# Performance work log

Hardware: AMD Instinct MI355X
Metric: run time of the kernel (lower is better)

Reference implementation:

```python
import jax, jax.numpy as jnp
import numpy as np

D_MODEL = 1024
N_HEADS = 16
HEAD_DIM = D_MODEL // N_HEADS
B, T = 2, 2048


def setup_inputs() -> dict:
    key = jax.random.key(0)
    ks = jax.random.split(key, 6)
    x = jax.random.normal(ks[0], (B, T, D_MODEL), dtype=jnp.float32)
    tgt_key_padding_mask = jnp.zeros((B, T), dtype=bool)
    scale = 0.02
    Wq = jax.random.normal(ks[1], (D_MODEL, D_MODEL), dtype=jnp.float32) * scale
    Wk = jax.random.normal(ks[2], (D_MODEL, D_MODEL), dtype=jnp.float32) * scale
    Wv = jax.random.normal(ks[3], (D_MODEL, D_MODEL), dtype=jnp.float32) * scale
    Wo = jax.random.normal(ks[4], (D_MODEL, D_MODEL), dtype=jnp.float32) * scale
    return {"x": x, "tgt_key_padding_mask": tgt_key_padding_mask,
            "Wq": Wq, "Wk": Wk, "Wv": Wv, "Wo": Wo}


def reference(x, tgt_key_padding_mask, Wq, Wk, Wv, Wo):
    # Eval-mode (dropout disabled) masked causal MHA, faithful to torch module.
    b, t, c = x.shape
    h, d = N_HEADS, HEAD_DIM
    # nn.Linear(bias=False): y = x @ W.T
    Q = (x @ Wq.T).reshape(b, t, h, d).transpose(0, 2, 1, 3)  # [B,H,T,d]
    K = (x @ Wk.T).reshape(b, t, h, d).transpose(0, 2, 1, 3)
    V = (x @ Wv.T).reshape(b, t, h, d).transpose(0, 2, 1, 3)
    scores = jnp.einsum('bhqd,bhkd->bhqk', Q, K) / jnp.sqrt(jnp.float32(d))
    # causal mask: True above the diagonal -> -inf
    cmask = jnp.triu(jnp.ones((t, t), dtype=bool), k=1)  # [T,T]
    neg_inf = jnp.float32(-jnp.inf)
    scores = jnp.where(cmask[None, None, :, :], neg_inf, scores)
    # key padding mask: [B,T] True=PAD, broadcast over query dim
    pmask = tgt_key_padding_mask[:, None, None, :]  # [B,1,1,T]
    scores = jnp.where(pmask, neg_inf, scores)
    attn = jax.nn.softmax(scores, axis=-1)
    out = jnp.einsum('bhqk,bhkd->bhqd', attn, V)  # [B,H,T,d]
    out = out.transpose(0, 2, 1, 3).reshape(b, t, c)
    out = out @ Wo.T
    return out
```

## Files before the change

### kernel.cpp

```cpp
#include <hip/hip_runtime.h>
#include <hip/hip_bf16.h>
#include <stdint.h>

#define D_MODEL 1024
#define NHEADS  16
#define HDIM    64
#define BB      2
#define TT      2048
#define MROWS   (BB*TT)
#define GK      1024

typedef __bf16 bf16_8 __attribute__((ext_vector_type(8)));
typedef __bf16 bf16_4 __attribute__((ext_vector_type(4)));
typedef float  f32x4  __attribute__((ext_vector_type(4)));
typedef unsigned short u16;

__device__ __forceinline__ u16 f2bf(float f) {
    union { float f; uint32_t u; } c; c.f = f;
    uint32_t u = c.u;
    uint32_t r = (u + 0x7FFFu + ((u >> 16) & 1u)) >> 16;
    return (u16)r;
}
__device__ __forceinline__ uint32_t pk2bf(float a, float b) {
    return (uint32_t)f2bf(a) | ((uint32_t)f2bf(b) << 16);
}

__device__ __forceinline__ void gload16(const void* g, void* l) {
    __builtin_amdgcn_global_load_lds(
        (const __attribute__((address_space(1))) unsigned int*)g,
        (__attribute__((address_space(3))) unsigned int*)l,
        16, 0, 0);
}

__global__ __launch_bounds__(256) void cvtk(
    const float* __restrict__ x,  const float* __restrict__ wq,
    const float* __restrict__ wk, const float* __restrict__ wv,
    const float* __restrict__ wo, const unsigned char* __restrict__ mk,
    u16* __restrict__ xb,  u16* __restrict__ wqb, u16* __restrict__ wkb,
    u16* __restrict__ wvb, u16* __restrict__ wob, uint32_t* __restrict__ pmb)
{
    int z = blockIdx.y;
    if (z == 5) {
        int gi = blockIdx.x*256 + threadIdx.x;
        if (gi < BB*TT/32) {
            uint32_t wv = 0;
            #pragma unroll
            for (int j = 0; j < 32; ++j)
                wv |= (mk[gi*32 + j] ? 1u : 0u) << j;
            pmb[gi] = wv;
        }
        return;
    }
    const float* in; u16* out; int n4;
    switch (z) {
        case 0: in = x;  out = xb;  n4 = MROWS*D_MODEL/4; break;
        case 1: in = wq; out = wqb; n4 = D_MODEL*D_MODEL/4; break;
        case 2: in = wk; out = wkb; n4 = D_MODEL*D_MODEL/4; break;
        case 3: in = wv; out = wvb; n4 = D_MODEL*D_MODEL/4; break;
        default: in = wo; out = wob; n4 = D_MODEL*D_MODEL/4; break;
    }
    for (int i = blockIdx.x*256 + threadIdx.x; i < n4; i += 1024*256) {
        float4 v = ((const float4*)in)[i];
        uint2 pk;
        pk.x = pk2bf(v.x, v.y);
        pk.y = pk2bf(v.z, v.w);
        ((uint2*)out)[i] = pk;
    }
}

template<int MODE>
__device__ __forceinline__ void gemm_body(
    const u16* __restrict__ A, const u16* __restrict__ Bm,
    void* __restrict__ dst, float oscale)
{
    __shared__ u16 As[128*64];
    __shared__ u16 Bs[128*64];
    const int tid  = threadIdx.x;
    const int lane = tid & 63, w = tid >> 6;
    const int wr = w >> 1, wc = w & 1;
    const int g = lane >> 4, lr = lane & 15;
    const int xcd = blockIdx.x & 7, qq_ = blockIdx.x >> 3;
    const int bn = qq_ & 7, bm = (qq_ >> 3)*8 + xcd;
    const int m0 = bm * 128, n0 = bn * 128;

    f32x4 acc[4][4];
    #pragma unroll
    for (int i = 0; i < 4; ++i)
        #pragma unroll
        for (int j = 0; j < 4; ++j)
            acc[i][j] = f32x4{0.f, 0.f, 0.f, 0.f};

    for (int kt = 0; kt < 16; ++kt) {
        int k0 = kt*64;
        #pragma unroll
        for (int r = 0; r < 4; ++r) {
            int o   = r*256 + tid;
            int row = o >> 3;
            int lc  = (o & 7) ^ (row & 7);
            gload16(A  + (size_t)(m0+row)*GK + k0 + lc*8,
                    (char*)As + (size_t)(r*256 + w*64)*16);
            gload16(Bm + (size_t)(n0+row)*GK + k0 + lc*8,
                    (char*)Bs + (size_t)(r*256 + w*64)*16);
        }
        __syncthreads();
        #pragma unroll
        for (int ks = 0; ks < 2; ++ks) {
            bf16_8 af[4], bfr[4];
            #pragma unroll
            for (int mt = 0; mt < 4; ++mt) {
                int row = wr*64 + mt*16 + lr;
                int ch  = (ks*4 + g) ^ (row & 7);
                af[mt] = *(const bf16_8*)((const char*)As + row*128 + ch*16);
            }
            #pragma unroll
            for (int nt = 0; nt < 4; ++nt) {
                int row = wc*64 + nt*16 + lr;
                int ch  = (ks*4 + g) ^ (row & 7);
                bfr[nt] = *(const bf16_8*)((const char*)Bs + row*128 + ch*16);
            }
            #pragma unroll
            for (int mt = 0; mt < 4; ++mt)
                #pragma unroll
                for (int nt = 0; nt < 4; ++nt) {
                    if (MODE == 1)
                        acc[mt][nt] = __builtin_amdgcn_mfma_f32_16x16x32_bf16(
                            bfr[nt], af[mt], acc[mt][nt], 0, 0, 0);
                    else
                        acc[mt][nt] = __builtin_amdgcn_mfma_f32_16x16x32_bf16(
                            af[mt], bfr[nt], acc[mt][nt], 0, 0, 0);
                }
        }
        __syncthreads();
    }

    #pragma unroll
    for (int mt = 0; mt < 4; ++mt) {
        #pragma unroll
        for (int nt = 0; nt < 4; ++nt) {
            #pragma unroll
            for (int r = 0; r < 4; ++r) {
                float v = acc[mt][nt][r];
                if (MODE == 0) {
                    int row = m0 + wr*64 + mt*16 + g*4 + r;
                    int col = n0 + wc*64 + nt*16 + lr;
                    int b = row >> 11, t = row & (TT-1);
                    int h = col >> 6,  d = col & 63;
                    ((u16*)dst)[(((size_t)(b*NHEADS + h)*TT + t)*HDIM + d)] = f2bf(v*oscale);
                } else {
                    int nrow = n0 + wc*64 + nt*16 + g*4 + r;
                    int mcol = m0 + wr*64 + mt*16 + lr;
                    int h = nrow >> 6,  d = nrow & 63;
                    int b = mcol >> 11, t = mcol & (TT-1);
                    ((u16*)dst)[(((size_t)(b*NHEADS + h)*HDIM + d)*TT + t)] = f2bf(v);
                }
            }
        }
    }
}

__global__ __launch_bounds__(256) void gemm_qkv(
    const u16* __restrict__ xb,
    const u16* __restrict__ wqb, const u16* __restrict__ wkb, const u16* __restrict__ wvb,
    u16* __restrict__ Qb, u16* __restrict__ Kb, u16* __restrict__ VTb)
{
    int z = blockIdx.y;
    if (z == 0)      gemm_body<0>(xb, wqb, Qb, 0.18033688f);
    else if (z == 1) gemm_body<0>(xb, wkb, Kb, 1.0f);
    else             gemm_body<1>(xb, wvb, VTb, 1.0f);
}

__global__ __launch_bounds__(256) void gemm_out(
    const u16* __restrict__ AOb, const u16* __restrict__ wob, float* __restrict__ out)
{
    __shared__ u16 As[128*64];
    __shared__ u16 Bs[64*64];
    const int tid  = threadIdx.x;
    const int lane = tid & 63, w = tid >> 6;
    const int g = lane >> 4, lr = lane & 15;
    const int xcd = blockIdx.x & 7, q_ = blockIdx.x >> 3;
    const int bn = q_ & 15, bm = (q_ >> 4)*8 + xcd;
    const int m0 = bm * 128, n0 = bn * 64;

    f32x4 acc[2][4];
    #pragma unroll
    for (int i = 0; i < 2; ++i)
        #pragma unroll
        for (int j = 0; j < 4; ++j)
            acc[i][j] = f32x4{0.f, 0.f, 0.f, 0.f};

    for (int kt = 0; kt < 16; ++kt) {
        int k0 = kt*64;
        #pragma unroll
        for (int r = 0; r < 4; ++r) {
            int o   = r*256 + tid;
            int row = o >> 3;
            int lc  = (o & 7) ^ (row & 7);
            gload16(AOb + (size_t)(m0+row)*GK + k0 + lc*8,
                    (char*)As + (size_t)(r*256 + w*64)*16);
        }
        #pragma unroll
        for (int r = 0; r < 2; ++r) {
            int o   = r*256 + tid;
            int row = o >> 3;
            int lc  = (o & 7) ^ (row & 7);
            gload16(wob + (size_t)(n0+row)*GK + k0 + lc*8,
                    (char*)Bs + (size_t)(r*256 + w*64)*16);
        }
        __syncthreads();
        #pragma unroll
        for (int ks = 0; ks < 2; ++ks) {
            bf16_8 af[2], bfr[4];
            #pragma unroll
            for (int mt = 0; mt < 2; ++mt) {
                int row = w*32 + mt*16 + lr;
                int ch  = (ks*4 + g) ^ (row & 7);
                af[mt] = *(const bf16_8*)((const char*)As + row*128 + ch*16);
            }
            #pragma unroll
            for (int nt = 0; nt < 4; ++nt) {
                int row = nt*16 + lr;
                int ch  = (ks*4 + g) ^ (row & 7);
                bfr[nt] = *(const bf16_8*)((const char*)Bs + row*128 + ch*16);
            }
            #pragma unroll
            for (int mt = 0; mt < 2; ++mt)
                #pragma unroll
                for (int nt = 0; nt < 4; ++nt)
                    acc[mt][nt] = __builtin_amdgcn_mfma_f32_16x16x32_bf16(
                        af[mt], bfr[nt], acc[mt][nt], 0, 0, 0);
        }
        __syncthreads();
    }

    #pragma unroll
    for (int mt = 0; mt < 2; ++mt)
        #pragma unroll
        for (int nt = 0; nt < 4; ++nt)
            #pragma unroll
            for (int r = 0; r < 4; ++r) {
                int row = m0 + w*32 + mt*16 + g*4 + r;
                int col = n0 + nt*16 + lr;
                out[(size_t)row*D_MODEL + col] = acc[mt][nt][r];
            }
}

__global__ __launch_bounds__(512, 4) void attn_fwd(
    const u16* __restrict__ Qb, const u16* __restrict__ Kb,
    const u16* __restrict__ VTb, const uint32_t* __restrict__ pmb,
    u16* __restrict__ AO)
{
    __shared__ u16 Ks[3][64*64];
    __shared__ u16 Vs[2][64*64];
    __shared__ u16 Pl[8][1152];
    __shared__ uint32_t Ml[64];

    const int tid = threadIdx.x, lane = tid & 63, w = tid >> 6;
    const int g = lane >> 4, lr = lane & 15;
    const int bh = blockIdx.x, yb = blockIdx.y;
    const int p  = (yb < 8) ? yb : 23 - yb;
    const int b = bh >> 4, h = bh & 15;
    const int qtH = 31 - p;
    const bool heavy = (w < 4);
    const int qlo = heavy ? (qtH*64 + w*16) : (p*64 + (w-4)*16);
    const int ta  = heavy ? qtH : p;
    const int nt  = qtH + 1;

    const u16* Qh = Qb  + (size_t)bh*TT*HDIM;
    const u16* Kh = Kb  + (size_t)bh*TT*HDIM;
    const u16* Vh = VTb + (size_t)bh*HDIM*TT;
    char* Pw = (char*)&Pl[w][0];

    if (tid < 64) Ml[tid] = pmb[b*(TT/32) + tid];

    bf16_8 qf[2];
    #pragma unroll
    for (int dc = 0; dc < 2; ++dc)
        qf[dc] = *(const bf16_8*)(Qh + (size_t)(qlo+lr)*HDIM + dc*32 + g*8);

    f32x4 o[4];
    #pragma unroll
    for (int i = 0; i < 4; ++i) o[i] = f32x4{0.f, 0.f, 0.f, 0.f};
    float l_run = 0.f;

    auto STAGE_K = [&](int t, int buf) {
        int kv0 = t*64;
        int row = tid >> 3;
        int lc  = (tid & 7) ^ (row & 7);
        gload16(Kh + (size_t)(kv0+row)*HDIM + lc*8,
                (char*)&Ks[buf][0] + (size_t)(w*64)*16);
    };
    auto STAGE_V = [&](int t, int buf) {
        int kv0 = t*64;
        int row = tid >> 3;
        int lc  = (tid & 7) ^ (row & 7);
        gload16(Vh + (size_t)row*TT + kv0 + lc*8,
                (char*)&Vs[buf][0] + (size_t)(w*64)*16);
    };

    STAGE_K(0, 0);
    STAGE_V(0, 0);
    STAGE_K(1, 1);

    int kb = 0;
    for (int t = 0; t < nt; ++t) {
        if (t + 1 < nt) asm volatile("s_waitcnt vmcnt(1) lgkmcnt(0)" ::: "memory");
        else            asm volatile("s_waitcnt vmcnt(0) lgkmcnt(0)" ::: "memory");
        __builtin_amdgcn_s_barrier();
        if (t + 1 < nt) STAGE_V(t+1, (t+1) & 1);
        if (t + 2 < nt) { int nk = kb + 2; if (nk >= 3) nk -= 3; STAGE_K(t+2, nk); }

        if (t <= ta) {
            const int kv0 = t*64;
            const u16* Kc = &Ks[kb][0];
            const u16* Vc = &Vs[t & 1][0];

            f32x4 s[4];
            __builtin_amdgcn_s_setprio(1);
            #pragma unroll
            for (int kvb = 0; kvb < 4; ++kvb) {
                int row = kvb*16 + lr;
                int sw  = row & 7;
                bf16_8 k0 = *(const bf16_8*)(Kc + row*64 + ((g    ) ^ sw)*8);
                bf16_8 k1 = *(const bf16_8*)(Kc + row*64 + ((4 + g) ^ sw)*8);
                f32x4 z = f32x4{0.f, 0.f, 0.f, 0.f};
                z = __builtin_amdgcn_mfma_f32_16x16x32_bf16(k0, qf[0], z, 0, 0, 0);
                z = __builtin_amdgcn_mfma_f32_16x16x32_bf16(k1, qf[1], z, 0, 0, 0);
                s[kvb] = z;
            }
            __builtin_amdgcn_s_setprio(0);

            bf16_8 vf[4][2];
            #pragma unroll
            for (int dt = 0; dt < 4; ++dt)
                #pragma unroll
                for (int hh = 0; hh < 2; ++hh)
                    vf[dt][hh] = *(const bf16_8*)(Vc + (dt*16+lr)*64 + ((hh*4+g) ^ (lr&7))*8);

            uint64_t m64 = (uint64_t)Ml[2*t] | ((uint64_t)Ml[2*t+1] << 32);
            if (m64) {
                #pragma unroll
                for (int kvb = 0; kvb < 4; ++kvb) {
                    uint32_t nib = (uint32_t)(m64 >> (kvb*16 + 4*g)) & 0xFu;
                    #pragma unroll
                    for (int r = 0; r < 4; ++r)
                        if ((nib >> r) & 1) s[kvb][r] = -1e30f;
                }
            }
            if (t == ta) {
                int q = qlo + lr;
                #pragma unroll
                for (int kvb = 0; kvb < 4; ++kvb) {
                    int kvb0 = kv0 + kvb*16 + 4*g;
                    #pragma unroll
                    for (int r = 0; r < 4; ++r)
                        if (kvb0 + r > q) s[kvb][r] = -1e30f;
                }
            }

            #pragma unroll
            for (int kvb = 0; kvb < 4; ++kvb)
                #pragma unroll
                for (int r = 0; r < 4; ++r)
                    s[kvb][r] = __builtin_amdgcn_exp2f(fminf(s[kvb][r], 80.f));
            float p0 = (s[0][0] + s[0][1]) + (s[0][2] + s[0][3]);
            float p1 = (s[1][0] + s[1][1]) + (s[1][2] + s[1][3]);
            float p2 = (s[2][0] + s[2][1]) + (s[2][2] + s[2][3]);
            float p3 = (s[3][0] + s[3][1]) + (s[3][2] + s[3][3]);
            float ps = (p0 + p1) + (p2 + p3);
            ps += __shfl_xor(ps, 16);
            ps += __shfl_xor(ps, 32);
            l_run += ps;

            #pragma unroll
            for (int kvb = 0; kvb < 4; ++kvb) {
                bf16_4 pk;
                pk[0] = (__bf16)s[kvb][0]; pk[1] = (__bf16)s[kvb][1];
                pk[2] = (__bf16)s[kvb][2]; pk[3] = (__bf16)s[kvb][3];
                *(bf16_4*)(Pw + lr*144 + kvb*32 + g*8) = pk;
            }
            asm volatile("s_waitcnt lgkmcnt(0)" ::: "memory");
            __builtin_amdgcn_sched_barrier(0);

            __builtin_amdgcn_s_setprio(1);
            #pragma unroll
            for (int hh = 0; hh < 2; ++hh) {
                bf16_8 pa = *(const bf16_8*)(Pw + lr*144 + hh*64 + g*16);
                #pragma unroll
                for (int dt = 0; dt < 4; ++dt)
                    o[dt] = __builtin_amdgcn_mfma_f32_16x16x32_bf16(
                        vf[dt][hh], pa, o[dt], 0, 0, 0);
            }
            __builtin_amdgcn_s_setprio(0);
        }

        ++kb; if (kb == 3) kb = 0;
    }

    float linv = (l_run > 0.f) ? 1.f/l_run : 0.f;
    u16* ot = (u16*)Pw;
    #pragma unroll
    for (int dt = 0; dt < 4; ++dt)
        #pragma unroll
        for (int r = 0; r < 4; ++r)
            ot[(dt*16 + 4*g + r)*17 + lr] = f2bf(o[dt][r]*linv);
    asm volatile("s_waitcnt lgkmcnt(0)" ::: "memory");
    __builtin_amdgcn_sched_barrier(0);
    #pragma unroll
    for (int qq = 0; qq < 16; ++qq)
        AO[((size_t)(b*TT + qlo + qq))*D_MODEL + h*HDIM + lane] = ot[lane*17 + qq];
}

extern "C" void kernel_launch(void* const* d_in, const int* in_sizes, int n_in,
                              void* d_out, int out_size, void* d_ws, size_t ws_size,
                              hipStream_t stream)
{
    const float* x  = (const float*)d_in[0];
    const unsigned char* mask = (const unsigned char*)d_in[1];
    const float* Wq = (const float*)d_in[2];
    const float* Wk = (const float*)d_in[3];
    const float* Wv = (const float*)d_in[4];
    const float* Wo = (const float*)d_in[5];
    float* out = (float*)d_out;

    char* ws = (char*)d_ws;
    u16* xb  = (u16*)(ws + 0);
    u16* wqb = (u16*)(ws + 8388608);
    u16* wkb = (u16*)(ws + 10485760);
    u16* wvb = (u16*)(ws + 12582912);
    u16* wob = (u16*)(ws + 14680064);
    u16* Qb  = (u16*)(ws + 16777216);
    u16* Kb  = (u16*)(ws + 25165824);
    u16* VTb = (u16*)(ws + 33554432);
    uint32_t* pmb = (uint32_t*)(ws + 41943040);
    u16* AOb = xb;

    cvtk<<<dim3(1024, 6), 256, 0, stream>>>(x, Wq, Wk, Wv, Wo, mask,
                                            xb, wqb, wkb, wvb, wob, pmb);
    gemm_qkv<<<dim3(256, 3), 256, 0, stream>>>(xb, wqb, wkb, wvb, Qb, Kb, VTb);
    attn_fwd<<<dim3(32, 16), 512, 0, stream>>>(Qb, Kb, VTb, pmb, AOb);
    gemm_out<<<dim3(512), 256, 0, stream>>>(AOb, wob, out);
}
```

Baseline: 106.2 us.

## Fuse Q/K/V projections into one GEMM sharing the x tile across three weights

```diff
diff --git a/kernel.cpp b/kernel.cpp
--- a/kernel.cpp
+++ b/kernel.cpp
@@ -68,105 +68,104 @@
     }
 }
 
-template<int MODE>
-__device__ __forceinline__ void gemm_body(
-    const u16* __restrict__ A, const u16* __restrict__ Bm,
-    void* __restrict__ dst, float oscale)
-{
-    __shared__ u16 As[128*64];
-    __shared__ u16 Bs[128*64];
-    const int tid  = threadIdx.x;
-    const int lane = tid & 63, w = tid >> 6;
-    const int wr = w >> 1, wc = w & 1;
-    const int g = lane >> 4, lr = lane & 15;
-    const int xcd = blockIdx.x & 7, qq_ = blockIdx.x >> 3;
-    const int bn = qq_ & 7, bm = (qq_ >> 3)*8 + xcd;
-    const int m0 = bm * 128, n0 = bn * 128;
-
-    f32x4 acc[4][4];
-    #pragma unroll
-    for (int i = 0; i < 4; ++i)
-        #pragma unroll
-        for (int j = 0; j < 4; ++j)
-            acc[i][j] = f32x4{0.f, 0.f, 0.f, 0.f};
-
-    for (int kt = 0; kt < 16; ++kt) {
-        int k0 = kt*64;
-        #pragma unroll
-        for (int r = 0; r < 4; ++r) {
-            int o   = r*256 + tid;
-            int row = o >> 3;
-            int lc  = (o & 7) ^ (row & 7);
-            gload16(A  + (size_t)(m0+row)*GK + k0 + lc*8,
-                    (char*)As + (size_t)(r*256 + w*64)*16);
-            gload16(Bm + (size_t)(n0+row)*GK + k0 + lc*8,
-                    (char*)Bs + (size_t)(r*256 + w*64)*16);
-        }
-        __syncthreads();
-        #pragma unroll
-        for (int ks = 0; ks < 2; ++ks) {
-            bf16_8 af[4], bfr[4];
-            #pragma unroll
-            for (int mt = 0; mt < 4; ++mt) {
-                int row = wr*64 + mt*16 + lr;
-                int ch  = (ks*4 + g) ^ (row & 7);
-                af[mt] = *(const bf16_8*)((const char*)As + row*128 + ch*16);
-            }
-            #pragma unroll
-            for (int nt = 0; nt < 4; ++nt) {
-                int row = wc*64 + nt*16 + lr;
-                int ch  = (ks*4 + g) ^ (row & 7);
-                bfr[nt] = *(const bf16_8*)((const char*)Bs + row*128 + ch*16);
-            }
-            #pragma unroll
-            for (int mt = 0; mt < 4; ++mt)
-                #pragma unroll
-                for (int nt = 0; nt < 4; ++nt) {
-                    if (MODE == 1)
-                        acc[mt][nt] = __builtin_amdgcn_mfma_f32_16x16x32_bf16(
-                            bfr[nt], af[mt], acc[mt][nt], 0, 0, 0);
-                    else
-                        acc[mt][nt] = __builtin_amdgcn_mfma_f32_16x16x32_bf16(
-                            af[mt], bfr[nt], acc[mt][nt], 0, 0, 0);
-                }
-        }
-        __syncthreads();
-    }
-
-    #pragma unroll
-    for (int mt = 0; mt < 4; ++mt) {
-        #pragma unroll
-        for (int nt = 0; nt < 4; ++nt) {
-            #pragma unroll
-            for (int r = 0; r < 4; ++r) {
-                float v = acc[mt][nt][r];
-                if (MODE == 0) {
-                    int row = m0 + wr*64 + mt*16 + g*4 + r;
-                    int col = n0 + wc*64 + nt*16 + lr;
-                    int b = row >> 11, t = row & (TT-1);
-                    int h = col >> 6,  d = col & 63;
-                    ((u16*)dst)[(((size_t)(b*NHEADS + h)*TT + t)*HDIM + d)] = f2bf(v*oscale);
-                } else {
-                    int nrow = n0 + wc*64 + nt*16 + g*4 + r;
-                    int mcol = m0 + wr*64 + mt*16 + lr;
-                    int h = nrow >> 6,  d = nrow & 63;
-                    int b = mcol >> 11, t = mcol & (TT-1);
-                    ((u16*)dst)[(((size_t)(b*NHEADS + h)*HDIM + d)*TT + t)] = f2bf(v);
-                }
-            }
-        }
-    }
-}
-
 __global__ __launch_bounds__(256) void gemm_qkv(
     const u16* __restrict__ xb,
     const u16* __restrict__ wqb, const u16* __restrict__ wkb, const u16* __restrict__ wvb,
     u16* __restrict__ Qb, u16* __restrict__ Kb, u16* __restrict__ VTb)
 {
-    int z = blockIdx.y;
-    if (z == 0)      gemm_body<0>(xb, wqb, Qb, 0.18033688f);
-    else if (z == 1) gemm_body<0>(xb, wkb, Kb, 1.0f);
-    else             gemm_body<1>(xb, wvb, VTb, 1.0f);
+    __shared__ u16 As[128*64];
+    __shared__ u16 Bs[3][64*64];
+    const int tid  = threadIdx.x;
+    const int lane = tid & 63, w = tid >> 6;
+    const int g = lane >> 4, lr = lane & 15;
+    const int xcd = blockIdx.x & 7, q_ = blockIdx.x >> 3;
+    const int bn = q_ & 15, bm = (q_ >> 4)*8 + xcd;
+    const int m0 = bm * 128, n0 = bn * 64;
+    const u16* Wz[3] = { wqb, wkb, wvb };
+
+    f32x4 acc[3][2][4];
+    #pragma unroll
+    for (int z = 0; z < 3; ++z)
+        #pragma unroll
+        for (int i = 0; i < 2; ++i)
+            #pragma unroll
+            for (int j = 0; j < 4; ++j)
+                acc[z][i][j] = f32x4{0.f, 0.f, 0.f, 0.f};
+
+    for (int kt = 0; kt < 16; ++kt) {
+        int k0 = kt*64;
+        #pragma unroll
+        for (int r = 0; r < 4; ++r) {
+            int o   = r*256 + tid;
+            int row = o >> 3;
+            int lc  = (o & 7) ^ (row & 7);
+            gload16(xb + (size_t)(m0+row)*GK + k0 + lc*8,
+                    (char*)As + (size_t)(r*256 + w*64)*16);
+        }
+        #pragma unroll
+        for (int z = 0; z < 3; ++z)
+            #pragma unroll
+            for (int r = 0; r < 2; ++r) {
+                int o   = r*256 + tid;
+                int row = o >> 3;
+                int lc  = (o & 7) ^ (row & 7);
+                gload16(Wz[z] + (size_t)(n0+row)*GK + k0 + lc*8,
+                        (char*)&Bs[z][0] + (size_t)(r*256 + w*64)*16);
+            }
+        __syncthreads();
+        #pragma unroll
+        for (int ks = 0; ks < 2; ++ks) {
+            bf16_8 af[2];
+            #pragma unroll
+            for (int mt = 0; mt < 2; ++mt) {
+                int row = w*32 + mt*16 + lr;
+                int ch  = (ks*4 + g) ^ (row & 7);
+                af[mt] = *(const bf16_8*)((const char*)As + row*128 + ch*16);
+            }
+            #pragma unroll
+            for (int z = 0; z < 3; ++z) {
+                bf16_8 bfr[4];
+                #pragma unroll
+                for (int nt = 0; nt < 4; ++nt) {
+                    int row = nt*16 + lr;
+                    int ch  = (ks*4 + g) ^ (row & 7);
+                    bfr[nt] = *(const bf16_8*)((const char*)&Bs[z][0] + row*128 + ch*16);
+                }
+                #pragma unroll
+                for (int mt = 0; mt < 2; ++mt)
+                    #pragma unroll
+                    for (int nt = 0; nt < 4; ++nt) {
+                        if (z == 2)
+                            acc[2][mt][nt] = __builtin_amdgcn_mfma_f32_16x16x32_bf16(
+                                bfr[nt], af[mt], acc[2][mt][nt], 0, 0, 0);
+                        else
+                            acc[z][mt][nt] = __builtin_amdgcn_mfma_f32_16x16x32_bf16(
+                                af[mt], bfr[nt], acc[z][mt][nt], 0, 0, 0);
+                    }
+            }
+        }
+        __syncthreads();
+    }
+
+    #pragma unroll
+    for (int mt = 0; mt < 2; ++mt)
+        #pragma unroll
+        for (int nt = 0; nt < 4; ++nt)
+            #pragma unroll
+            for (int r = 0; r < 4; ++r) {
+                int row = m0 + w*32 + mt*16 + g*4 + r;
+                int col = n0 + nt*16 + lr;
+                int b = row >> 11, t = row & (TT-1);
+                int h = col >> 6,  d = col & 63;
+                size_t qi = (((size_t)(b*NHEADS + h)*TT + t)*HDIM + d);
+                Qb[qi] = f2bf(acc[0][mt][nt][r] * 0.18033688f);
+                Kb[qi] = f2bf(acc[1][mt][nt][r]);
+                int nrow = n0 + nt*16 + g*4 + r;
+                int mcol = m0 + w*32 + mt*16 + lr;
+                int hv = nrow >> 6,  dv = nrow & 63;
+                int bv = mcol >> 11, tv = mcol & (TT-1);
+                VTb[(((size_t)(bv*NHEADS + hv)*HDIM + dv)*TT + tv)] = f2bf(acc[2][mt][nt][r]);
+            }
 }
 
 __global__ __launch_bounds__(256) void gemm_out(
@@ -436,7 +435,7 @@
 
     cvtk<<<dim3(1024, 6), 256, 0, stream>>>(x, Wq, Wk, Wv, Wo, mask,
                                             xb, wqb, wkb, wvb, wob, pmb);
-    gemm_qkv<<<dim3(256, 3), 256, 0, stream>>>(xb, wqb, wkb, wvb, Qb, Kb, VTb);
+    gemm_qkv<<<dim3(512), 256, 0, stream>>>(xb, wqb, wkb, wvb, Qb, Kb, VTb);
     attn_fwd<<<dim3(32, 16), 512, 0, stream>>>(Qb, Kb, VTb, pmb, AOb);
     gemm_out<<<dim3(512), 256, 0, stream>>>(AOb, wob, out);
 }
```

New measurement: 98.79 us. 1.08x faster.
